# Performance work log

Hardware: AMD Instinct MI355X
Metric: run time of the kernel (lower is better)

## Reference

```python
import jax, jax.numpy as jnp
import numpy as np

N, E, DIN, H0, H1, HEADS = 50000, 600000, 128, 64, 64, 4
NEG_SLOPE = 0.2
BN_EPS = 1e-5


def setup_inputs() -> dict:
    key = jax.random.key(0)
    ks = iter(jax.random.split(key, 40))
    def p(shape, s=0.05):
        return jax.random.normal(next(ks), shape, jnp.float32) * s
    inp = {}
    inp['x'] = jax.random.normal(next(ks), (N, DIN), jnp.float32)
    inp['edge_index'] = jax.random.randint(next(ks), (2, E), 0, N, dtype=jnp.int32)
    inp['gcn1_w'] = p((DIN, H0)); inp['gcn1_b'] = p((H0,))
    inp['gcn2_w'] = p((H0, H1)); inp['gcn2_b'] = p((H1,))
    inp['gat1_w'] = p((DIN, HEADS * H0))
    inp['gat1_asrc'] = p((HEADS, H0)); inp['gat1_adst'] = p((HEADS, H0))
    inp['gat1_b'] = p((HEADS * H0,))
    inp['gat2_w'] = p((HEADS * H0, H1))
    inp['gat2_asrc'] = p((1, H1)); inp['gat2_adst'] = p((1, H1))
    inp['gat2_b'] = p((H1,))
    inp['sage1_wl'] = p((DIN, H0)); inp['sage1_bl'] = p((H0,)); inp['sage1_wr'] = p((DIN, H0))
    inp['sage2_wl'] = p((H0, H1)); inp['sage2_bl'] = p((H1,)); inp['sage2_wr'] = p((H0, H1))
    inp['bn_gcn_g'] = jnp.ones((H1,), jnp.float32); inp['bn_gcn_b'] = jnp.zeros((H1,), jnp.float32)
    inp['bn_gat_g'] = jnp.ones((H1,), jnp.float32); inp['bn_gat_b'] = jnp.zeros((H1,), jnp.float32)
    inp['bn_sage_g'] = jnp.ones((H1,), jnp.float32); inp['bn_sage_b'] = jnp.zeros((H1,), jnp.float32)
    inp['fc1_w'] = p((3 * H1, H1)); inp['fc1_b'] = p((H1,))
    inp['fc2_w'] = p((H1, 2)); inp['fc2_b'] = p((2,))
    return inp


def _gcn(x, w, b, src, dst, n):
    h = x @ w
    loop = jnp.arange(n)
    s = jnp.concatenate([src, loop]); d = jnp.concatenate([dst, loop])
    deg = jax.ops.segment_sum(jnp.ones(d.shape, h.dtype), d, n)
    dinv = jax.lax.rsqrt(jnp.maximum(deg, 1.0))  # deg >= 1 due to self-loops
    norm = dinv[s] * dinv[d]
    out = jax.ops.segment_sum(h[s] * norm[:, None], d, n)
    return out + b


def _gat(x, w, asrc, adst, b, src, dst, n, heads, outc, concat):
    # GATConv with self-loops; per-destination softmax over incoming edges
    h = (x @ w).reshape(n, heads, outc)
    loop = jnp.arange(n)
    s = jnp.concatenate([src, loop]); d = jnp.concatenate([dst, loop])
    a_s = jnp.einsum('nhc,hc->nh', h, asrc)
    a_d = jnp.einsum('nhc,hc->nh', h, adst)
    e = a_s[s] + a_d[d]                           # [Etot, H]
    e = jnp.where(e > 0, e, NEG_SLOPE * e)        # leaky relu
    emax = jax.ops.segment_max(e, d, n)           # every node has a self-loop
    ex = jnp.exp(e - emax[d])
    denom = jax.ops.segment_sum(ex, d, n)
    alpha = ex / (denom[d] + 1e-16)               # [Etot, H]
    out = jax.ops.segment_sum(h[s] * alpha[:, :, None], d, n)  # [n, H, C]
    out = out.reshape(n, heads * outc) if concat else out.mean(axis=1)
    return out + b


def _sage(x, wl, bl, wr, src, dst, n):
    # SAGEConv (mean aggr): lin_l(mean_j x_j) + lin_r(x_i)
    deg = jax.ops.segment_sum(jnp.ones(src.shape, x.dtype), dst, n)
    agg = jax.ops.segment_sum(x[src], dst, n) / jnp.maximum(deg, 1.0)[:, None]
    return agg @ wl + bl + x @ wr


def _bn(x, g, b):
    m = x.mean(0)
    v = x.var(0)
    return (x - m) * jax.lax.rsqrt(v + BN_EPS) * g + b


def reference(x, edge_index, gcn1_w, gcn1_b, gcn2_w, gcn2_b,
              gat1_w, gat1_asrc, gat1_adst, gat1_b,
              gat2_w, gat2_asrc, gat2_adst, gat2_b,
              sage1_wl, sage1_bl, sage1_wr, sage2_wl, sage2_bl, sage2_wr,
              bn_gcn_g, bn_gcn_b, bn_gat_g, bn_gat_b, bn_sage_g, bn_sage_b,
              fc1_w, fc1_b, fc2_w, fc2_b):
    src, dst = edge_index[0], edge_index[1]
    n = x.shape[0]
    g = jax.nn.relu(_gcn(x, gcn1_w, gcn1_b, src, dst, n))
    g = _bn(jax.nn.relu(_gcn(g, gcn2_w, gcn2_b, src, dst, n)), bn_gcn_g, bn_gcn_b)
    a = jax.nn.elu(_gat(x, gat1_w, gat1_asrc, gat1_adst, gat1_b, src, dst, n, HEADS, H0, True))
    a = _bn(jax.nn.elu(_gat(a, gat2_w, gat2_asrc, gat2_adst, gat2_b, src, dst, n, 1, H1, False)), bn_gat_g, bn_gat_b)
    s = jax.nn.relu(_sage(x, sage1_wl, sage1_bl, sage1_wr, src, dst, n))
    s = _bn(jax.nn.relu(_sage(s, sage2_wl, sage2_bl, sage2_wr, src, dst, n)), bn_sage_g, bn_sage_b)
    out = jnp.concatenate([g, a, s], axis=-1)
    h = jax.nn.relu(out @ fc1_w + fc1_b)
    return h @ fc2_w + fc2_b
```

## Files before the change

kernel.cpp:

```cpp
#include <hip/hip_runtime.h>
#include <math.h>

#define NEG_SLOPE 0.2f
#define BN_EPS 1e-5f

typedef short short8 __attribute__((ext_vector_type(8)));
typedef float floatx16 __attribute__((ext_vector_type(16)));

__device__ __forceinline__ float d_leaky(float x){ return x > 0.f ? x : NEG_SLOPE * x; }
__device__ __forceinline__ float d_elu(float x){ return x > 0.f ? x : expm1f(x); }

__device__ __forceinline__ unsigned short f2bf_rne(float f){
  unsigned int u = __float_as_uint(f);
  unsigned int r = (u + 0x7fffu + ((u >> 16) & 1u)) >> 16;
  return (unsigned short)r;
}
__device__ __forceinline__ float bf2f(unsigned short h){ return __uint_as_float((unsigned int)h << 16); }
__device__ __forceinline__ float2 bf2x(unsigned int u){
  float2 r;
  r.x = __uint_as_float(u << 16);
  r.y = __uint_as_float(u & 0xffff0000u);
  return r;
}

__device__ __forceinline__ float wave_sum(float v){
  #pragma unroll
  for (int off = 32; off > 0; off >>= 1) v += __shfl_xor(v, off, 64);
  return v;
}
__device__ __forceinline__ int wave_scan_incl(int v, int lane){
  #pragma unroll
  for (int off = 1; off < 64; off <<= 1){
    int u = __shfl_up(v, off, 64);
    if (lane >= off) v += u;
  }
  return v;
}

__global__ void k_count(const int* __restrict__ dst, int* __restrict__ deg, int E){
  int e = blockIdx.x * blockDim.x + threadIdx.x;
  if (e < E) atomicAdd(&deg[dst[e]], 1);
}

__global__ __launch_bounds__(256) void k_scan_a(const int* __restrict__ deg, int* __restrict__ bsum, int n){
  int t = threadIdx.x;
  int base = blockIdx.x * 1024 + t * 4;
  int d0=0,d1=0,d2=0,d3=0;
  if (base + 3 < n){ int4 v = *(const int4*)(deg + base); d0=v.x; d1=v.y; d2=v.z; d3=v.w; }
  else {
    if (base   < n) d0 = deg[base];
    if (base+1 < n) d1 = deg[base+1];
    if (base+2 < n) d2 = deg[base+2];
    if (base+3 < n) d3 = deg[base+3];
  }
  int s = d0+d1+d2+d3;
  __shared__ int wsm[4];
  int lane = t & 63, w = t >> 6;
  int incl = wave_scan_incl(s, lane);
  if (lane == 63) wsm[w] = incl;
  __syncthreads();
  if (t == 0) bsum[blockIdx.x] = wsm[0]+wsm[1]+wsm[2]+wsm[3];
}

__global__ void k_scan_b(int* __restrict__ bsum, int* __restrict__ rowp, int nb, int n){
  int t = threadIdx.x;
  int v = (t < nb) ? bsum[t] : 0;
  int incl = wave_scan_incl(v, t);
  if (t < nb) bsum[t] = incl - v;
  if (t == 63) rowp[n] = incl;
}

__global__ __launch_bounds__(256) void k_scan_c(const int* __restrict__ deg, const int* __restrict__ bsum,
                                                int* __restrict__ rowp, float* __restrict__ dinv,
                                                float* __restrict__ sdinv, int n){
  int t = threadIdx.x;
  int base = blockIdx.x * 1024 + t * 4;
  int d0=0,d1=0,d2=0,d3=0;
  if (base + 3 < n){ int4 v = *(const int4*)(deg + base); d0=v.x; d1=v.y; d2=v.z; d3=v.w; }
  else {
    if (base   < n) d0 = deg[base];
    if (base+1 < n) d1 = deg[base+1];
    if (base+2 < n) d2 = deg[base+2];
    if (base+3 < n) d3 = deg[base+3];
  }
  int s = d0+d1+d2+d3;
  __shared__ int wsm[4];
  int lane = t & 63, w = t >> 6;
  int incl = wave_scan_incl(s, lane);
  if (lane == 63) wsm[w] = incl;
  __syncthreads();
  int woff = 0;
  #pragma unroll
  for (int j = 0; j < 4; j++) if (j < w) woff += wsm[j];
  int r = bsum[blockIdx.x] + woff + incl - s;
  int dd[4] = {d0,d1,d2,d3};
  #pragma unroll
  for (int j = 0; j < 4; j++){
    int i = base + j;
    if (i < n){
      rowp[i] = r;
      dinv[i] = rsqrtf((float)(dd[j] + 1));
      sdinv[i] = 1.0f / fmaxf((float)dd[j], 1.0f);
    }
    r += dd[j];
  }
}

__global__ void k_scatter(const int* __restrict__ src, const int* __restrict__ dst,
                          const int* __restrict__ rowp, int* __restrict__ fill,
                          int* __restrict__ colv, int* __restrict__ dstv, int E){
  int e = blockIdx.x * blockDim.x + threadIdx.x;
  if (e < E){
    int d = dst[e];
    int pos = rowp[d] + atomicAdd(&fill[d], 1);
    colv[pos] = src[e];
    dstv[pos] = d;
  }
}

__global__ void k_asplit(const float* __restrict__ a, unsigned short* __restrict__ h,
                         unsigned short* __restrict__ l, int total){
  int i = blockIdx.x * blockDim.x + threadIdx.x;
  if (i < total){
    float v = a[i];
    unsigned short hh = f2bf_rne(v);
    h[i] = hh;
    l[i] = f2bf_rne(v - bf2f(hh));
  }
}

struct WDesc { const float* w; unsigned short* th; unsigned short* tl; int K; int Nc; int perm; };
struct WPack { WDesc d[8]; };
__global__ void k_wsplit(WPack p){
  WDesc w = p.d[blockIdx.y];
  int total = w.K * w.Nc;
  for (int i = blockIdx.x * blockDim.x + threadIdx.x; i < total; i += gridDim.x * blockDim.x){
    int k = i / w.Nc, n = i % w.Nc;
    int kd = (w.perm == 1) ? ((k & 63) * 4 + (k >> 6)) : k;
    int nd = (w.perm == 2) ? (((n & 63) << 2) | (n >> 6)) : n;
    float v = w.w[i];
    unsigned short h = f2bf_rne(v);
    w.th[(size_t)nd * w.K + kd] = h;
    w.tl[(size_t)nd * w.K + kd] = f2bf_rne(v - bf2f(h));
  }
}

__device__ __forceinline__ void gemm_term(floatx16& acc0, floatx16& acc1,
    const unsigned short* __restrict__ Ah, const unsigned short* __restrict__ Al,
    const unsigned short* __restrict__ Bh, const unsigned short* __restrict__ Bl,
    int K, int lda, int arow, int lr, int ko8){
  const unsigned short* ap  = Ah + (size_t)arow * lda + ko8;
  const unsigned short* alp = Al ? Al + (size_t)arow * lda + ko8 : nullptr;
  const unsigned short* bh0 = Bh + (size_t)lr * K + ko8;
  const unsigned short* bl0 = Bl + (size_t)lr * K + ko8;
  const unsigned short* bh1 = bh0 + (size_t)32 * K;
  const unsigned short* bl1 = bl0 + (size_t)32 * K;
  for (int k0 = 0; k0 < K; k0 += 16){
    short8 a  = *(const short8*)(ap + k0);
    short8 h0 = *(const short8*)(bh0 + k0);
    short8 l0 = *(const short8*)(bl0 + k0);
    short8 h1 = *(const short8*)(bh1 + k0);
    short8 l1 = *(const short8*)(bl1 + k0);
    if (alp){
      short8 a2 = *(const short8*)(alp + k0);
      acc0 = __builtin_amdgcn_mfma_f32_32x32x16_bf16(a2, h0, acc0, 0, 0, 0);
      acc1 = __builtin_amdgcn_mfma_f32_32x32x16_bf16(a2, h1, acc1, 0, 0, 0);
    }
    acc0 = __builtin_amdgcn_mfma_f32_32x32x16_bf16(a, l0, acc0, 0, 0, 0);
    acc0 = __builtin_amdgcn_mfma_f32_32x32x16_bf16(a, h0, acc0, 0, 0, 0);
    acc1 = __builtin_amdgcn_mfma_f32_32x32x16_bf16(a, l1, acc1, 0, 0, 0);
    acc1 = __builtin_amdgcn_mfma_f32_32x32x16_bf16(a, h1, acc1, 0, 0, 0);
  }
}

struct BDesc {
  const unsigned short *A1h, *A1l, *B1h, *B1l;
  const unsigned short *A2h, *A2l, *B2h, *B2l;
  int K1, lda1, K2, lda2;
  const float* bias;
  unsigned short* out; int ldc, coloff, act;
  const float* fc2w; const float* fc2b; float* outf;
};
struct BPack { BDesc d[3]; };
__global__ __launch_bounds__(256) void k_gemm_b(BPack p, int M){
  BDesc d = p.d[blockIdx.y];
  int wave = threadIdx.x >> 6, lane = threadIdx.x & 63;
  int m0 = blockIdx.x * 128 + wave * 32;
  int lr = lane & 31;
  int ko8 = (lane >> 5) * 8;
  floatx16 acc0 = {0,0,0,0,0,0,0,0,0,0,0,0,0,0,0,0};
  floatx16 acc1 = {0,0,0,0,0,0,0,0,0,0,0,0,0,0,0,0};
  int arow = m0 + lr; if (arow >= M) arow = M - 1;
  gemm_term(acc0, acc1, d.A1h, d.A1l, d.B1h, d.B1l, d.K1, d.lda1, arow, lr, ko8);
  if (d.K2) gemm_term(acc0, acc1, d.A2h, d.A2l, d.B2h, d.B2l, d.K2, d.lda2, arow, lr, ko8);
  int col0 = lr, col1 = lr + 32;
  float bias0 = d.bias ? d.bias[col0] : 0.f;
  float bias1 = d.bias ? d.bias[col1] : 0.f;
  float w00 = 0.f, w01 = 0.f, w10 = 0.f, w11 = 0.f;
  if (d.fc2w){
    w00 = d.fc2w[col0 * 2 + 0]; w01 = d.fc2w[col0 * 2 + 1];
    w10 = d.fc2w[col1 * 2 + 0]; w11 = d.fc2w[col1 * 2 + 1];
  }
  int rbase = m0 + 4 * (lane >> 5);
  #pragma unroll
  for (int reg = 0; reg < 16; reg++){
    int row = rbase + (reg & 3) + 8 * (reg >> 2);
    float v0 = acc0[reg] + bias0;
    float v1 = acc1[reg] + bias1;
    if (d.act){ v0 = fmaxf(v0, 0.f); v1 = fmaxf(v1, 0.f); }
    if (d.out && row < M){
      d.out[(size_t)row * d.ldc + d.coloff + col0] = f2bf_rne(v0);
      d.out[(size_t)row * d.ldc + d.coloff + col1] = f2bf_rne(v1);
    }
    if (d.fc2w){
      float p0 = v0 * w00 + v1 * w10;
      float p1 = v0 * w01 + v1 * w11;
      #pragma unroll
      for (int off = 16; off > 0; off >>= 1){
        p0 += __shfl_xor(p0, off, 64);
        p1 += __shfl_xor(p1, off, 64);
      }
      if ((lane & 31) == 0 && row < M){
        d.outf[(size_t)row * 2 + 0] = p0 + d.fc2b[0];
        d.outf[(size_t)row * 2 + 1] = p1 + d.fc2b[1];
      }
    }
  }
}

__global__ __launch_bounds__(256) void k_gemm320(
    const unsigned short* __restrict__ Ah, const unsigned short* __restrict__ Al,
    const unsigned short* __restrict__ Bh, const unsigned short* __restrict__ Bl,
    unsigned short* __restrict__ C1, unsigned short* __restrict__ C2, int M)
{
  const int K = 128;
  int wave = threadIdx.x >> 6, lane = threadIdx.x & 63;
  int m0 = blockIdx.x * 128 + wave * 32;
  int n0 = blockIdx.y * 64;
  int lr = lane & 31;
  int ko8 = (lane >> 5) * 8;
  floatx16 acc0 = {0,0,0,0,0,0,0,0,0,0,0,0,0,0,0,0};
  floatx16 acc1 = {0,0,0,0,0,0,0,0,0,0,0,0,0,0,0,0};
  int arow = m0 + lr; if (arow >= M) arow = M - 1;
  const unsigned short* ap_h = Ah + (size_t)arow * K + ko8;
  const unsigned short* ap_l = Al + (size_t)arow * K + ko8;
  const unsigned short* bp_h0 = Bh + (size_t)(n0 + lr) * K + ko8;
  const unsigned short* bp_l0 = Bl + (size_t)(n0 + lr) * K + ko8;
  const unsigned short* bp_h1 = bp_h0 + (size_t)32 * K;
  const unsigned short* bp_l1 = bp_l0 + (size_t)32 * K;
  for (int k0 = 0; k0 < K; k0 += 16){
    short8 a_h  = *(const short8*)(ap_h + k0);
    short8 a_l  = *(const short8*)(ap_l + k0);
    short8 b_h0 = *(const short8*)(bp_h0 + k0);
    short8 b_l0 = *(const short8*)(bp_l0 + k0);
    short8 b_h1 = *(const short8*)(bp_h1 + k0);
    short8 b_l1 = *(const short8*)(bp_l1 + k0);
    acc0 = __builtin_amdgcn_mfma_f32_32x32x16_bf16(a_l, b_h0, acc0, 0, 0, 0);
    acc0 = __builtin_amdgcn_mfma_f32_32x32x16_bf16(a_h, b_l0, acc0, 0, 0, 0);
    acc0 = __builtin_amdgcn_mfma_f32_32x32x16_bf16(a_h, b_h0, acc0, 0, 0, 0);
    acc1 = __builtin_amdgcn_mfma_f32_32x32x16_bf16(a_l, b_h1, acc1, 0, 0, 0);
    acc1 = __builtin_amdgcn_mfma_f32_32x32x16_bf16(a_h, b_l1, acc1, 0, 0, 0);
    acc1 = __builtin_amdgcn_mfma_f32_32x32x16_bf16(a_h, b_h1, acc1, 0, 0, 0);
  }
  int col0 = n0 + lr, col1 = col0 + 32;
  unsigned short* Cp; int ld, c0, c1;
  if (col0 >= 256){ Cp = C2; ld = 64; c0 = col0 - 256; c1 = col1 - 256; }
  else { Cp = C1; ld = 256; c0 = col0; c1 = col1; }
  int rbase = m0 + 4 * (lane >> 5);
  #pragma unroll
  for (int reg = 0; reg < 16; reg++){
    int row = rbase + (reg & 3) + 8 * (reg >> 2);
    if (row >= M) continue;
    Cp[(size_t)row * ld + c0] = f2bf_rne(acc0[reg]);
    Cp[(size_t)row * ld + c1] = f2bf_rne(acc1[reg]);
  }
}

__global__ __launch_bounds__(256) void k_gat_attn4(
    const unsigned short* __restrict__ h, const float* __restrict__ asrc,
    const float* __restrict__ adst, float* __restrict__ a_s, float* __restrict__ a_d, int n){
  int node = blockIdx.x * 4 + (threadIdx.x >> 6);
  int c = threadIdx.x & 63;
  if (node >= n) return;
  uint2 u = *(const uint2*)(h + (size_t)node * 256 + c * 4);
  float2 p0 = bf2x(u.x), p1 = bf2x(u.y);
  float s0 = wave_sum(p0.x * asrc[c]);
  float s1 = wave_sum(p0.y * asrc[64 + c]);
  float s2 = wave_sum(p1.x * asrc[128 + c]);
  float s3 = wave_sum(p1.y * asrc[192 + c]);
  float d0 = wave_sum(p0.x * adst[c]);
  float d1 = wave_sum(p0.y * adst[64 + c]);
  float d2 = wave_sum(p1.x * adst[128 + c]);
  float d3 = wave_sum(p1.y * adst[192 + c]);
  if (c == 0){
    *(float4*)(a_s + (size_t)node * 4) = make_float4(s0, s1, s2, s3);
    *(float4*)(a_d + (size_t)node * 4) = make_float4(d0, d1, d2, d3);
  }
}

__global__ __launch_bounds__(256) void k_gat_attn1(
    const unsigned short* __restrict__ h, int ld, const float* __restrict__ asrc,
    const float* __restrict__ adst, float* __restrict__ a_s, float* __restrict__ a_d, int n){
  int node = blockIdx.x * 4 + (threadIdx.x >> 6);
  int c = threadIdx.x & 63;
  if (node >= n) return;
  float v = bf2f(h[(size_t)node * ld + c]);
  float s = wave_sum(v * asrc[c]);
  float d = wave_sum(v * adst[c]);
  if (c == 0){ a_s[node] = s; a_d[node] = d; }
}

__global__ void k_edge_w4(const int* __restrict__ colv, const int* __restrict__ dstv,
                          const float* __restrict__ a_s, const float* __restrict__ a_d,
                          unsigned short* __restrict__ w4b, int E){
  int i = blockIdx.x * blockDim.x + threadIdx.x;
  if (i >= E) return;
  float4 s4 = *(const float4*)(a_s + (size_t)colv[i] * 4);
  float4 d4 = *(const float4*)(a_d + (size_t)dstv[i] * 4);
  float w0 = __expf(d_leaky(s4.x + d4.x));
  float w1 = __expf(d_leaky(s4.y + d4.y));
  float w2 = __expf(d_leaky(s4.z + d4.z));
  float w3 = __expf(d_leaky(s4.w + d4.w));
  uint2 q;
  q.x = (unsigned int)f2bf_rne(w0) | ((unsigned int)f2bf_rne(w1) << 16);
  q.y = (unsigned int)f2bf_rne(w2) | ((unsigned int)f2bf_rne(w3) << 16);
  *(uint2*)(w4b + (size_t)i * 4) = q;
}

__global__ void k_edge_w1(const int* __restrict__ colv, const int* __restrict__ dstv,
                          const float* __restrict__ a_s, const float* __restrict__ a_d,
                          float* __restrict__ w1, int E){
  int i = blockIdx.x * blockDim.x + threadIdx.x;
  if (i >= E) return;
  w1[i] = __expf(d_leaky(a_s[colv[i]] + a_d[dstv[i]]));
}

__global__ __launch_bounds__(256) void k_l1agg(
    const unsigned short* __restrict__ gath, const unsigned short* __restrict__ xh,
    const unsigned short* __restrict__ g1h,
    const int* __restrict__ rowp, const int* __restrict__ colv,
    const unsigned short* __restrict__ w4b,
    const float* __restrict__ a_s, const float* __restrict__ a_d,
    const float* __restrict__ gat1_b, const float* __restrict__ gcn1_b,
    const float* __restrict__ dinv, const float* __restrict__ sdinv,
    unsigned short* __restrict__ oh, unsigned short* __restrict__ g2h,
    unsigned short* __restrict__ aggXh, int n)
{
  int node = blockIdx.x * 4 + (threadIdx.x >> 6);
  int c = threadIdx.x & 63;
  if (node >= n) return;
  float4 asn = *(const float4*)(a_s + (size_t)node * 4);
  float4 adn = *(const float4*)(a_d + (size_t)node * 4);
  float ws0 = __expf(d_leaky(asn.x + adn.x));
  float ws1 = __expf(d_leaky(asn.y + adn.y));
  float ws2 = __expf(d_leaky(asn.z + adn.z));
  float ws3 = __expf(d_leaky(asn.w + adn.w));
  uint2 su = *(const uint2*)(gath + (size_t)node * 256 + c * 4);
  float2 sp0 = bf2x(su.x), sp1 = bf2x(su.y);
  float den0 = ws0, den1 = ws1, den2 = ws2, den3 = ws3;
  float acc0 = ws0 * sp0.x, acc1 = ws1 * sp0.y, acc2 = ws2 * sp1.x, acc3 = ws3 * sp1.y;
  float di = dinv[node];
  float gacc = di * bf2f(g1h[(size_t)node * 64 + c]);
  float sx0 = 0.f, sx1 = 0.f;
  int b = rowp[node], e = rowp[node + 1];
  for (int i = b; i < e; i += 8){
    int idx[8]; float mm[8]; int s[8];
    #pragma unroll
    for (int j = 0; j < 8; j++){
      int t = i + j;
      mm[j] = (t < e) ? 1.f : 0.f;
      idx[j] = (t < e) ? t : (e - 1);
    }
    #pragma unroll
    for (int j = 0; j < 8; j++) s[j] = colv[idx[j]];
    uint2 wq[8];
    #pragma unroll
    for (int j = 0; j < 8; j++) wq[j] = *(const uint2*)(w4b + (size_t)idx[j] * 4);
    uint2 hv[8];
    #pragma unroll
    for (int j = 0; j < 8; j++) hv[j] = *(const uint2*)(gath + (size_t)s[j] * 256 + c * 4);
    unsigned int hx[8];
    #pragma unroll
    for (int j = 0; j < 8; j++) hx[j] = *(const unsigned int*)(xh + (size_t)s[j] * 128 + c * 2);
    unsigned short hg[8];
    #pragma unroll
    for (int j = 0; j < 8; j++) hg[j] = g1h[(size_t)s[j] * 64 + c];
    float wd[8];
    #pragma unroll
    for (int j = 0; j < 8; j++) wd[j] = dinv[s[j]];
    #pragma unroll
    for (int j = 0; j < 8; j++){
      float m = mm[j];
      float2 w01 = bf2x(wq[j].x), w23 = bf2x(wq[j].y);
      float w0 = m * w01.x, w1 = m * w01.y, w2 = m * w23.x, w3 = m * w23.y;
      float2 a = bf2x(hv[j].x), bb = bf2x(hv[j].y);
      den0 += w0; den1 += w1; den2 += w2; den3 += w3;
      acc0 += w0 * a.x;  acc1 += w1 * a.y;
      acc2 += w2 * bb.x; acc3 += w3 * bb.y;
      gacc += m * wd[j] * bf2f(hg[j]);
      float2 p = bf2x(hx[j]);
      sx0 += m * p.x; sx1 += m * p.y;
    }
  }
  float v0 = d_elu(acc0 / (den0 + 1e-16f) + gat1_b[c]);
  float v1 = d_elu(acc1 / (den1 + 1e-16f) + gat1_b[64 + c]);
  float v2 = d_elu(acc2 / (den2 + 1e-16f) + gat1_b[128 + c]);
  float v3 = d_elu(acc3 / (den3 + 1e-16f) + gat1_b[192 + c]);
  uint2 ohv;
  ohv.x = (unsigned int)f2bf_rne(v0) | ((unsigned int)f2bf_rne(v1) << 16);
  ohv.y = (unsigned int)f2bf_rne(v2) | ((unsigned int)f2bf_rne(v3) << 16);
  *(uint2*)(oh + (size_t)node * 256 + c * 4) = ohv;
  g2h[(size_t)node * 64 + c] = f2bf_rne(fmaxf(di * gacc + gcn1_b[c], 0.f));
  float sd = sdinv[node];
  *(unsigned int*)(aggXh + (size_t)node * 128 + c * 2) =
      (unsigned int)f2bf_rne(sx0 * sd) | ((unsigned int)f2bf_rne(sx1 * sd) << 16);
}

__global__ __launch_bounds__(256) void k_f2(
    const unsigned short* __restrict__ m192,
    const int* __restrict__ rowp, const int* __restrict__ colv,
    const float* __restrict__ w1, const float* __restrict__ a_s, const float* __restrict__ a_d,
    const float* __restrict__ dinv, const float* __restrict__ sdinv,
    const float* __restrict__ gat2_b, const float* __restrict__ gcn2_b,
    unsigned short* __restrict__ cat,
    unsigned short* __restrict__ aggSh,
    int n){
  int node = blockIdx.x * 4 + (threadIdx.x >> 6);
  int c = threadIdx.x & 63;
  if (node >= n) return;
  float di = dinv[node];
  const unsigned short* srow = m192 + (size_t)node * 192;
  float tden = __expf(d_leaky(a_s[node] + a_d[node]));
  float tacc = tden * bf2f(srow[c]);
  float gacc = di * bf2f(srow[64 + c]);
  float sacc = 0.f;
  int b = rowp[node], e = rowp[node + 1];
  for (int i = b; i < e; i += 8){
    int idx[8]; float mm[8]; int s[8];
    #pragma unroll
    for (int j = 0; j < 8; j++){
      int t = i + j;
      mm[j] = (t < e) ? 1.f : 0.f;
      idx[j] = (t < e) ? t : (e - 1);
    }
    #pragma unroll
    for (int j = 0; j < 8; j++) s[j] = colv[idx[j]];
    float w[8];
    #pragma unroll
    for (int j = 0; j < 8; j++) w[j] = w1[idx[j]] * mm[j];
    unsigned short ht[8], hg[8], hs[8];
    #pragma unroll
    for (int j = 0; j < 8; j++){
      const unsigned short* r = m192 + (size_t)s[j] * 192;
      ht[j] = r[c]; hg[j] = r[64 + c]; hs[j] = r[128 + c];
    }
    float wd[8];
    #pragma unroll
    for (int j = 0; j < 8; j++) wd[j] = dinv[s[j]];
    #pragma unroll
    for (int j = 0; j < 8; j++){
      tden += w[j]; tacc += w[j] * bf2f(ht[j]);
      gacc += mm[j] * wd[j] * bf2f(hg[j]);
      sacc += mm[j] * bf2f(hs[j]);
    }
  }
  cat[(size_t)node * 192 + 64 + c] = f2bf_rne(d_elu(tacc / (tden + 1e-16f) + gat2_b[c]));
  cat[(size_t)node * 192 + c] = f2bf_rne(fmaxf(di * gacc + gcn2_b[c], 0.f));
  aggSh[(size_t)node * 64 + c] = f2bf_rne(sacc * sdinv[node]);
}

__global__ void k_bn_stats3(const unsigned short* __restrict__ x,
                            float* __restrict__ bnGCN, float* __restrict__ bnGAT,
                            float* __restrict__ bnSAGE, int n){
  int seg = blockIdx.y;
  float* sums = (seg == 0) ? bnGCN : (seg == 1) ? bnGAT : bnSAGE;
  int co = seg * 64;
  int c = threadIdx.x & 63;
  int rl = threadIdx.x >> 6;
  float s = 0.f, q = 0.f;
  for (int r = blockIdx.x * 4 + rl; r < n; r += gridDim.x * 4){
    float v = bf2f(x[(size_t)r * 192 + co + c]);
    s += v; q += v * v;
  }
  __shared__ float ls[4][64], lq[4][64];
  ls[rl][c] = s; lq[rl][c] = q;
  __syncthreads();
  if (rl == 0){
    s = ls[0][c] + ls[1][c] + ls[2][c] + ls[3][c];
    q = lq[0][c] + lq[1][c] + lq[2][c] + lq[3][c];
    atomicAdd(&sums[c], s);
    atomicAdd(&sums[64 + c], q);
  }
}

__global__ __launch_bounds__(256) void k_bnfold(
    const float* __restrict__ bnGCN, const float* __restrict__ bnGAT, const float* __restrict__ bnSAGE,
    const float* __restrict__ gg, const float* __restrict__ gb,
    const float* __restrict__ ag, const float* __restrict__ ab,
    const float* __restrict__ sg, const float* __restrict__ sb,
    const float* __restrict__ w, const float* __restrict__ wb, float nf,
    unsigned short* __restrict__ fwh, unsigned short* __restrict__ fwl, float* __restrict__ fb)
{
  int tid = threadIdx.x;
  auto st = [&](int c, float& s, float& t){
    int cc = c & 63;
    const float *bn, *g, *b;
    if (c < 64){ bn = bnGCN; g = gg; b = gb; }
    else if (c < 128){ bn = bnGAT; g = ag; b = ab; }
    else { bn = bnSAGE; g = sg; b = sb; }
    float m = bn[cc] / nf;
    float var = bn[64 + cc] / nf - m * m;
    float inv = rsqrtf(var + BN_EPS);
    s = inv * g[cc];
    t = b[cc] - m * inv * g[cc];
  };
  if (tid < 64){
    float acc = wb[tid];
    for (int c = 0; c < 192; c++){
      float s, t; st(c, s, t);
      acc += t * w[c * 64 + tid];
    }
    fb[tid] = acc;
  }
  for (int i = tid; i < 192 * 64; i += 256){
    int c = i >> 6, nn = i & 63;
    float s, t; st(c, s, t);
    float v = s * w[i];
    unsigned short hh = f2bf_rne(v);
    fwh[nn * 192 + c] = hh;
    fwl[nn * 192 + c] = f2bf_rne(v - bf2f(hh));
  }
}

extern "C" void kernel_launch(void* const* d_in, const int* in_sizes, int n_in,
                              void* d_out, int out_size, void* d_ws, size_t ws_size,
                              hipStream_t stream){
  (void)n_in; (void)out_size; (void)ws_size;
  const float* x        = (const float*)d_in[0];
  const int*   ei       = (const int*)  d_in[1];
  const float* gcn1_w   = (const float*)d_in[2];
  const float* gcn1_b   = (const float*)d_in[3];
  const float* gcn2_w   = (const float*)d_in[4];
  const float* gcn2_b   = (const float*)d_in[5];
  const float* gat1_w   = (const float*)d_in[6];
  const float* gat1_as  = (const float*)d_in[7];
  const float* gat1_ad  = (const float*)d_in[8];
  const float* gat1_b   = (const float*)d_in[9];
  const float* gat2_w   = (const float*)d_in[10];
  const float* gat2_as  = (const float*)d_in[11];
  const float* gat2_ad  = (const float*)d_in[12];
  const float* gat2_b   = (const float*)d_in[13];
  const float* sage1_wl = (const float*)d_in[14];
  const float* sage1_bl = (const float*)d_in[15];
  const float* sage1_wr = (const float*)d_in[16];
  const float* sage2_wl = (const float*)d_in[17];
  const float* sage2_bl = (const float*)d_in[18];
  const float* sage2_wr = (const float*)d_in[19];
  const float* bn_gcn_g = (const float*)d_in[20];
  const float* bn_gcn_b = (const float*)d_in[21];
  const float* bn_gat_g = (const float*)d_in[22];
  const float* bn_gat_b = (const float*)d_in[23];
  const float* bn_sage_g= (const float*)d_in[24];
  const float* bn_sage_b= (const float*)d_in[25];
  const float* fc1_w    = (const float*)d_in[26];
  const float* fc1_b    = (const float*)d_in[27];
  const float* fc2_w    = (const float*)d_in[28];
  const float* fc2_b    = (const float*)d_in[29];
  float* out = (float*)d_out;

  const int N = in_sizes[0] / 128;
  const int E = in_sizes[1] / 2;
  const int* src = ei;
  const int* dst = ei + E;
  const int nb = (N + 1023) / 1024;

  char* ws = (char*)d_ws;
  size_t off = 0;
  auto alloc = [&](size_t bytes) -> void* {
    void* p = ws + off;
    off = (off + bytes + 255) & ~(size_t)255;
    return p;
  };
  char* zbase = (char*)alloc(0);
  int*   deg   = (int*)  alloc((size_t)N * 4);
  int*   fill  = (int*)  alloc((size_t)N * 4);
  float* bnA   = (float*)alloc(128 * 4);
  float* bnB   = (float*)alloc(128 * 4);
  float* bnC   = (float*)alloc(128 * 4);
  size_t zbytes = (size_t)((char*)alloc(0) - zbase);
  int*   rowp  = (int*)  alloc((size_t)(N + 1) * 4);
  int*   colv  = (int*)  alloc((size_t)E * 4);
  int*   dstv  = (int*)  alloc((size_t)E * 4);
  int*   bsum  = (int*)  alloc(64 * 4);
  float* dinv  = (float*)alloc((size_t)N * 4);
  float* sdinv = (float*)alloc((size_t)N * 4);
  float* as1   = (float*)alloc((size_t)N * 4 * 4);
  float* ad1   = (float*)alloc((size_t)N * 4 * 4);
  float* as2   = (float*)alloc((size_t)N * 4);
  float* ad2   = (float*)alloc((size_t)N * 4);
  unsigned short* w4b = (unsigned short*)alloc((size_t)E * 4 * 2);
  float* w1    = (float*)alloc((size_t)E * 4);
  unsigned short* xh    = (unsigned short*)alloc((size_t)N * 128 * 2);
  unsigned short* xl    = (unsigned short*)alloc((size_t)N * 128 * 2);
  unsigned short* gath  = (unsigned short*)alloc((size_t)N * 256 * 2);
  unsigned short* oh    = (unsigned short*)alloc((size_t)N * 256 * 2);
  unsigned short* g1h   = (unsigned short*)alloc((size_t)N * 64 * 2);
  unsigned short* g2h   = (unsigned short*)alloc((size_t)N * 64 * 2);
  unsigned short* aggXh = (unsigned short*)alloc((size_t)N * 128 * 2);
  unsigned short* aggSh = (unsigned short*)alloc((size_t)N * 64 * 2);
  unsigned short* m192  = (unsigned short*)alloc((size_t)N * 192 * 2);
  unsigned short* cath  = (unsigned short*)alloc((size_t)N * 192 * 2);
  unsigned short* b320h = (unsigned short*)alloc((size_t)320 * 128 * 2);
  unsigned short* b320l = (unsigned short*)alloc((size_t)320 * 128 * 2);
  unsigned short* gcn2h = (unsigned short*)alloc((size_t)64 * 64 * 2);
  unsigned short* gcn2l = (unsigned short*)alloc((size_t)64 * 64 * 2);
  unsigned short* gat2h = (unsigned short*)alloc((size_t)64 * 256 * 2);
  unsigned short* gat2l = (unsigned short*)alloc((size_t)64 * 256 * 2);
  unsigned short* s1wlh = (unsigned short*)alloc((size_t)64 * 128 * 2);
  unsigned short* s1wll = (unsigned short*)alloc((size_t)64 * 128 * 2);
  unsigned short* s1wrh = (unsigned short*)alloc((size_t)64 * 128 * 2);
  unsigned short* s1wrl = (unsigned short*)alloc((size_t)64 * 128 * 2);
  unsigned short* s2wlh = (unsigned short*)alloc((size_t)64 * 64 * 2);
  unsigned short* s2wll = (unsigned short*)alloc((size_t)64 * 64 * 2);
  unsigned short* s2wrh = (unsigned short*)alloc((size_t)64 * 64 * 2);
  unsigned short* s2wrl = (unsigned short*)alloc((size_t)64 * 64 * 2);
  unsigned short* fwh   = (unsigned short*)alloc((size_t)64 * 192 * 2);
  unsigned short* fwl   = (unsigned short*)alloc((size_t)64 * 192 * 2);
  float* fb             = (float*)alloc(64 * 4);

  hipMemsetAsync(zbase, 0, zbytes, stream);

  k_count <<<(E + 255) / 256, 256, 0, stream>>>(dst, deg, E);
  k_scan_a<<<nb, 256, 0, stream>>>(deg, bsum, N);
  k_scan_b<<<1, 64, 0, stream>>>(bsum, rowp, nb, N);
  k_scan_c<<<nb, 256, 0, stream>>>(deg, bsum, rowp, dinv, sdinv, N);
  k_scatter<<<(E + 255) / 256, 256, 0, stream>>>(src, dst, rowp, fill, colv, dstv, E);

  {
    WPack p;
    p.d[0] = {gat1_w, b320h, b320l, 128, 256, 2};
    p.d[1] = {gcn1_w, b320h + 256 * 128, b320l + 256 * 128, 128, 64, 0};
    p.d[2] = {gat2_w, gat2h, gat2l, 256, 64, 1};
    p.d[3] = {sage1_wl, s1wlh, s1wll, 128, 64, 0};
    p.d[4] = {sage1_wr, s1wrh, s1wrl, 128, 64, 0};
    p.d[5] = {sage2_wl, s2wlh, s2wll, 64, 64, 0};
    p.d[6] = {sage2_wr, s2wrh, s2wrl, 64, 64, 0};
    p.d[7] = {gcn2_w, gcn2h, gcn2l, 64, 64, 0};
    dim3 g(32, 8);
    k_wsplit<<<g, 256, 0, stream>>>(p);
  }
  k_asplit<<<(N * 128 + 255) / 256, 256, 0, stream>>>(x, xh, xl, N * 128);

  const int gx = (N + 127) / 128;
  const int gn = (N + 3) / 4;

  {
    dim3 g(gx, 5);
    k_gemm320<<<g, 256, 0, stream>>>(xh, xl, b320h, b320l, gath, g1h, N);
  }
  k_gat_attn4<<<gn, 256, 0, stream>>>(gath, gat1_as, gat1_ad, as1, ad1, N);
  k_edge_w4<<<(E + 255) / 256, 256, 0, stream>>>(colv, dstv, as1, ad1, w4b, E);
  k_l1agg<<<gn, 256, 0, stream>>>(gath, xh, g1h, rowp, colv, w4b, as1, ad1,
                                  gat1_b, gcn1_b, dinv, sdinv, oh, g2h, aggXh, N);

  {
    BPack p;
    p.d[0] = {oh, nullptr, gat2h, gat2l, nullptr, nullptr, nullptr, nullptr,
              256, 256, 0, 0, nullptr, m192, 192, 0, 0, nullptr, nullptr, nullptr};
    p.d[1] = {g2h, nullptr, gcn2h, gcn2l, nullptr, nullptr, nullptr, nullptr,
              64, 64, 0, 0, nullptr, m192, 192, 64, 0, nullptr, nullptr, nullptr};
    p.d[2] = {aggXh, nullptr, s1wlh, s1wll, xh, xl, s1wrh, s1wrl,
              128, 128, 128, 128, sage1_bl, m192, 192, 128, 1, nullptr, nullptr, nullptr};
    dim3 g(gx, 3);
    k_gemm_b<<<g, 256, 0, stream>>>(p, N);
  }
  k_gat_attn1<<<gn, 256, 0, stream>>>(m192, 192, gat2_as, gat2_ad, as2, ad2, N);
  k_edge_w1<<<(E + 255) / 256, 256, 0, stream>>>(colv, dstv, as2, ad2, w1, E);
  k_f2<<<gn, 256, 0, stream>>>(m192, rowp, colv, w1, as2, ad2, dinv, sdinv,
                               gat2_b, gcn2_b, cath, aggSh, N);

  {
    BPack p;
    p.d[0] = {aggSh, nullptr, s2wlh, s2wll, m192 + 128, nullptr, s2wrh, s2wrl,
              64, 64, 64, 192, sage2_bl, cath, 192, 128, 1, nullptr, nullptr, nullptr};
    p.d[1] = p.d[0]; p.d[2] = p.d[0];
    dim3 g(gx, 1);
    k_gemm_b<<<g, 256, 0, stream>>>(p, N);
  }

  {
    dim3 g(128, 3);
    k_bn_stats3<<<g, 256, 0, stream>>>(cath, bnB, bnA, bnC, N);
  }
  k_bnfold<<<1, 256, 0, stream>>>(bnB, bnA, bnC,
                                  bn_gcn_g, bn_gcn_b, bn_gat_g, bn_gat_b, bn_sage_g, bn_sage_b,
                                  fc1_w, fc1_b, (float)N, fwh, fwl, fb);

  {
    BPack p;
    p.d[0] = {cath, nullptr, fwh, fwl, nullptr, nullptr, nullptr, nullptr,
              192, 192, 0, 0, fb, nullptr, 64, 0, 1, fc2_w, fc2_b, out};
    p.d[1] = p.d[0]; p.d[2] = p.d[0];
    dim3 g(gx, 1);
    k_gemm_b<<<g, 256, 0, stream>>>(p, N);
  }
}
```

Baseline: 633.3 us.

## Fuse small kernels: scan, asplit, GAT2 attention, edge weights, BN fold

Cuts the launch count in several places. The single-block scan step moves into k_scan_c, which also seeds fill with row offsets so the scatter no longer reads rowp. The x bf16 split becomes an extra slot of k_wsplit. The GAT layer-2 attention dot products are computed in the GEMM epilogue through the fc2 path, and the edge weights are computed inline in k_f2 instead of in a separate edge kernel with its own buffer. BN statistics and the fold are merged with a last-block-done atomic counter. The trade-offs are more exp work inside the aggregation loop and extra global atomics and fences.

```diff
diff --git a/kernel.cpp b/kernel.cpp
--- a/kernel.cpp
+++ b/kernel.cpp
@@ -37,8 +37,11 @@
   return v;
 }
 
-__global__ void k_count(const int* __restrict__ dst, int* __restrict__ deg, int E){
+__global__ void k_count(const int* __restrict__ dst, int* __restrict__ deg, int E,
+                        const float* __restrict__ g2as, const float* __restrict__ g2ad,
+                        float* __restrict__ aw2){
   int e = blockIdx.x * blockDim.x + threadIdx.x;
+  if (e < 64){ aw2[e * 2 + 0] = g2as[e]; aw2[e * 2 + 1] = g2ad[e]; }
   if (e < E) atomicAdd(&deg[dst[e]], 1);
 }
 
@@ -62,18 +65,18 @@
   if (t == 0) bsum[blockIdx.x] = wsm[0]+wsm[1]+wsm[2]+wsm[3];
 }
 
-__global__ void k_scan_b(int* __restrict__ bsum, int* __restrict__ rowp, int nb, int n){
+__global__ __launch_bounds__(256) void k_scan_c(const int* __restrict__ deg, const int* __restrict__ bsum,
+                                                int* __restrict__ rowp, int* __restrict__ fill,
+                                                float* __restrict__ dinv,
+                                                float* __restrict__ sdinv, int n, int nb){
+  __shared__ int sbx[2];
   int t = threadIdx.x;
-  int v = (t < nb) ? bsum[t] : 0;
-  int incl = wave_scan_incl(v, t);
-  if (t < nb) bsum[t] = incl - v;
-  if (t == 63) rowp[n] = incl;
-}
-
-__global__ __launch_bounds__(256) void k_scan_c(const int* __restrict__ deg, const int* __restrict__ bsum,
-                                                int* __restrict__ rowp, float* __restrict__ dinv,
-                                                float* __restrict__ sdinv, int n){
-  int t = threadIdx.x;
+  if (t < 64){
+    int v = (t < nb) ? bsum[t] : 0;
+    int incl = wave_scan_incl(v, t);
+    if (t == (int)blockIdx.x) sbx[0] = incl - v;
+    if (t == 63) sbx[1] = incl;
+  }
   int base = blockIdx.x * 1024 + t * 4;
   int d0=0,d1=0,d2=0,d3=0;
   if (base + 3 < n){ int4 v = *(const int4*)(deg + base); d0=v.x; d1=v.y; d2=v.z; d3=v.w; }
@@ -92,48 +95,48 @@
   int woff = 0;
   #pragma unroll
   for (int j = 0; j < 4; j++) if (j < w) woff += wsm[j];
-  int r = bsum[blockIdx.x] + woff + incl - s;
+  int r = sbx[0] + woff + incl - s;
   int dd[4] = {d0,d1,d2,d3};
   #pragma unroll
   for (int j = 0; j < 4; j++){
     int i = base + j;
     if (i < n){
       rowp[i] = r;
+      fill[i] = r;
       dinv[i] = rsqrtf((float)(dd[j] + 1));
       sdinv[i] = 1.0f / fmaxf((float)dd[j], 1.0f);
     }
     r += dd[j];
   }
+  if (blockIdx.x == 0 && t == 0) rowp[n] = sbx[1];
 }
 
 __global__ void k_scatter(const int* __restrict__ src, const int* __restrict__ dst,
-                          const int* __restrict__ rowp, int* __restrict__ fill,
+                          int* __restrict__ fill,
                           int* __restrict__ colv, int* __restrict__ dstv, int E){
   int e = blockIdx.x * blockDim.x + threadIdx.x;
   if (e < E){
     int d = dst[e];
-    int pos = rowp[d] + atomicAdd(&fill[d], 1);
+    int pos = atomicAdd(&fill[d], 1);
     colv[pos] = src[e];
     dstv[pos] = d;
   }
 }
 
-__global__ void k_asplit(const float* __restrict__ a, unsigned short* __restrict__ h,
-                         unsigned short* __restrict__ l, int total){
-  int i = blockIdx.x * blockDim.x + threadIdx.x;
-  if (i < total){
-    float v = a[i];
-    unsigned short hh = f2bf_rne(v);
-    h[i] = hh;
-    l[i] = f2bf_rne(v - bf2f(hh));
-  }
-}
-
 struct WDesc { const float* w; unsigned short* th; unsigned short* tl; int K; int Nc; int perm; };
-struct WPack { WDesc d[8]; };
+struct WPack { WDesc d[9]; };
 __global__ void k_wsplit(WPack p){
   WDesc w = p.d[blockIdx.y];
   int total = w.K * w.Nc;
+  if (w.perm == 3){
+    for (int i = blockIdx.x * blockDim.x + threadIdx.x; i < total; i += gridDim.x * blockDim.x){
+      float v = w.w[i];
+      unsigned short h = f2bf_rne(v);
+      w.th[i] = h;
+      w.tl[i] = f2bf_rne(v - bf2f(h));
+    }
+    return;
+  }
   for (int i = blockIdx.x * blockDim.x + threadIdx.x; i < total; i += gridDim.x * blockDim.x){
     int k = i / w.Nc, n = i % w.Nc;
     int kd = (w.perm == 1) ? ((k & 63) * 4 + (k >> 6)) : k;
@@ -196,10 +199,11 @@
   int col0 = lr, col1 = lr + 32;
   float bias0 = d.bias ? d.bias[col0] : 0.f;
   float bias1 = d.bias ? d.bias[col1] : 0.f;
-  float w00 = 0.f, w01 = 0.f, w10 = 0.f, w11 = 0.f;
+  float w00 = 0.f, w01 = 0.f, w10 = 0.f, w11 = 0.f, fb0 = 0.f, fb1 = 0.f;
   if (d.fc2w){
     w00 = d.fc2w[col0 * 2 + 0]; w01 = d.fc2w[col0 * 2 + 1];
     w10 = d.fc2w[col1 * 2 + 0]; w11 = d.fc2w[col1 * 2 + 1];
+    if (d.fc2b){ fb0 = d.fc2b[0]; fb1 = d.fc2b[1]; }
   }
   int rbase = m0 + 4 * (lane >> 5);
   #pragma unroll
@@ -221,8 +225,8 @@
         p1 += __shfl_xor(p1, off, 64);
       }
       if ((lane & 31) == 0 && row < M){
-        d.outf[(size_t)row * 2 + 0] = p0 + d.fc2b[0];
-        d.outf[(size_t)row * 2 + 1] = p1 + d.fc2b[1];
+        d.outf[(size_t)row * 2 + 0] = p0 + fb0;
+        d.outf[(size_t)row * 2 + 1] = p1 + fb1;
       }
     }
   }
@@ -298,18 +302,6 @@
   }
 }
 
-__global__ __launch_bounds__(256) void k_gat_attn1(
-    const unsigned short* __restrict__ h, int ld, const float* __restrict__ asrc,
-    const float* __restrict__ adst, float* __restrict__ a_s, float* __restrict__ a_d, int n){
-  int node = blockIdx.x * 4 + (threadIdx.x >> 6);
-  int c = threadIdx.x & 63;
-  if (node >= n) return;
-  float v = bf2f(h[(size_t)node * ld + c]);
-  float s = wave_sum(v * asrc[c]);
-  float d = wave_sum(v * adst[c]);
-  if (c == 0){ a_s[node] = s; a_d[node] = d; }
-}
-
 __global__ void k_edge_w4(const int* __restrict__ colv, const int* __restrict__ dstv,
                           const float* __restrict__ a_s, const float* __restrict__ a_d,
                           unsigned short* __restrict__ w4b, int E){
@@ -325,14 +317,6 @@
   q.x = (unsigned int)f2bf_rne(w0) | ((unsigned int)f2bf_rne(w1) << 16);
   q.y = (unsigned int)f2bf_rne(w2) | ((unsigned int)f2bf_rne(w3) << 16);
   *(uint2*)(w4b + (size_t)i * 4) = q;
-}
-
-__global__ void k_edge_w1(const int* __restrict__ colv, const int* __restrict__ dstv,
-                          const float* __restrict__ a_s, const float* __restrict__ a_d,
-                          float* __restrict__ w1, int E){
-  int i = blockIdx.x * blockDim.x + threadIdx.x;
-  if (i >= E) return;
-  w1[i] = __expf(d_leaky(a_s[colv[i]] + a_d[dstv[i]]));
 }
 
 __global__ __launch_bounds__(256) void k_l1agg(
@@ -419,7 +403,7 @@
 __global__ __launch_bounds__(256) void k_f2(
     const unsigned short* __restrict__ m192,
     const int* __restrict__ rowp, const int* __restrict__ colv,
-    const float* __restrict__ w1, const float* __restrict__ a_s, const float* __restrict__ a_d,
+    const float* __restrict__ as2ad2,
     const float* __restrict__ dinv, const float* __restrict__ sdinv,
     const float* __restrict__ gat2_b, const float* __restrict__ gcn2_b,
     unsigned short* __restrict__ cat,
@@ -430,7 +414,8 @@
   if (node >= n) return;
   float di = dinv[node];
   const unsigned short* srow = m192 + (size_t)node * 192;
-  float tden = __expf(d_leaky(a_s[node] + a_d[node]));
+  float adn = as2ad2[node * 2 + 1];
+  float tden = __expf(d_leaky(as2ad2[node * 2 + 0] + adn));
   float tacc = tden * bf2f(srow[c]);
   float gacc = di * bf2f(srow[64 + c]);
   float sacc = 0.f;
@@ -447,7 +432,7 @@
     for (int j = 0; j < 8; j++) s[j] = colv[idx[j]];
     float w[8];
     #pragma unroll
-    for (int j = 0; j < 8; j++) w[j] = w1[idx[j]] * mm[j];
+    for (int j = 0; j < 8; j++) w[j] = mm[j] * __expf(d_leaky(as2ad2[(size_t)s[j] * 2] + adn));
     unsigned short ht[8], hg[8], hs[8];
     #pragma unroll
     for (int j = 0; j < 8; j++){
@@ -469,9 +454,16 @@
   aggSh[(size_t)node * 64 + c] = f2bf_rne(sacc * sdinv[node]);
 }
 
-__global__ void k_bn_stats3(const unsigned short* __restrict__ x,
-                            float* __restrict__ bnGCN, float* __restrict__ bnGAT,
-                            float* __restrict__ bnSAGE, int n){
+__global__ __launch_bounds__(256) void k_bn_stats_fold(
+    const unsigned short* __restrict__ x,
+    float* __restrict__ bnGCN, float* __restrict__ bnGAT, float* __restrict__ bnSAGE,
+    const float* __restrict__ gg, const float* __restrict__ gb,
+    const float* __restrict__ ag, const float* __restrict__ ab,
+    const float* __restrict__ sg, const float* __restrict__ sb,
+    const float* __restrict__ w, const float* __restrict__ wb, float nf,
+    unsigned short* __restrict__ fwh, unsigned short* __restrict__ fwl, float* __restrict__ fb,
+    int* __restrict__ done, int nblocks, int n)
+{
   int seg = blockIdx.y;
   float* sums = (seg == 0) ? bnGCN : (seg == 1) ? bnGAT : bnSAGE;
   int co = seg * 64;
@@ -491,44 +483,51 @@
     atomicAdd(&sums[c], s);
     atomicAdd(&sums[64 + c], q);
   }
-}
-
-__global__ __launch_bounds__(256) void k_bnfold(
-    const float* __restrict__ bnGCN, const float* __restrict__ bnGAT, const float* __restrict__ bnSAGE,
-    const float* __restrict__ gg, const float* __restrict__ gb,
-    const float* __restrict__ ag, const float* __restrict__ ab,
-    const float* __restrict__ sg, const float* __restrict__ sb,
-    const float* __restrict__ w, const float* __restrict__ wb, float nf,
-    unsigned short* __restrict__ fwh, unsigned short* __restrict__ fwl, float* __restrict__ fb)
-{
+  __syncthreads();
+  __shared__ int lastflag;
+  if (threadIdx.x == 0){
+    __threadfence();
+    int old = atomicAdd(done, 1);
+    lastflag = (old == nblocks - 1);
+  }
+  __syncthreads();
+  if (!lastflag) return;
+  __threadfence();
+  __shared__ float sbn[3][128];
+  for (int i = threadIdx.x; i < 384; i += 256){
+    float* p = (i < 128) ? bnGCN : (i < 256) ? bnGAT : bnSAGE;
+    sbn[i >> 7][i & 127] = atomicAdd(&p[i & 127], 0.0f);
+  }
+  __syncthreads();
   int tid = threadIdx.x;
-  auto st = [&](int c, float& s, float& t){
-    int cc = c & 63;
-    const float *bn, *g, *b;
-    if (c < 64){ bn = bnGCN; g = gg; b = gb; }
-    else if (c < 128){ bn = bnGAT; g = ag; b = ab; }
-    else { bn = bnSAGE; g = sg; b = sb; }
-    float m = bn[cc] / nf;
-    float var = bn[64 + cc] / nf - m * m;
+  auto st = [&](int c2, float& sc, float& tc){
+    int cc = c2 & 63;
+    int sg2 = c2 >> 6;
+    const float *g, *b;
+    if (sg2 == 0){ g = gg; b = gb; }
+    else if (sg2 == 1){ g = ag; b = ab; }
+    else { g = sg; b = sb; }
+    float m = sbn[sg2][cc] / nf;
+    float var = sbn[sg2][64 + cc] / nf - m * m;
     float inv = rsqrtf(var + BN_EPS);
-    s = inv * g[cc];
-    t = b[cc] - m * inv * g[cc];
+    sc = inv * g[cc];
+    tc = b[cc] - m * inv * g[cc];
   };
   if (tid < 64){
     float acc = wb[tid];
-    for (int c = 0; c < 192; c++){
-      float s, t; st(c, s, t);
-      acc += t * w[c * 64 + tid];
+    for (int c2 = 0; c2 < 192; c2++){
+      float sc, tc; st(c2, sc, tc);
+      acc += tc * w[c2 * 64 + tid];
     }
     fb[tid] = acc;
   }
   for (int i = tid; i < 192 * 64; i += 256){
-    int c = i >> 6, nn = i & 63;
-    float s, t; st(c, s, t);
-    float v = s * w[i];
+    int c2 = i >> 6, nn = i & 63;
+    float sc, tc; st(c2, sc, tc);
+    float v = sc * w[i];
     unsigned short hh = f2bf_rne(v);
-    fwh[nn * 192 + c] = hh;
-    fwl[nn * 192 + c] = f2bf_rne(v - bf2f(hh));
+    fwh[nn * 192 + c2] = hh;
+    fwl[nn * 192 + c2] = f2bf_rne(v - bf2f(hh));
   }
 }
 
@@ -583,12 +582,13 @@
   };
   char* zbase = (char*)alloc(0);
   int*   deg   = (int*)  alloc((size_t)N * 4);
-  int*   fill  = (int*)  alloc((size_t)N * 4);
   float* bnA   = (float*)alloc(128 * 4);
   float* bnB   = (float*)alloc(128 * 4);
   float* bnC   = (float*)alloc(128 * 4);
+  int*   done  = (int*)  alloc(4);
   size_t zbytes = (size_t)((char*)alloc(0) - zbase);
   int*   rowp  = (int*)  alloc((size_t)(N + 1) * 4);
+  int*   fill  = (int*)  alloc((size_t)N * 4);
   int*   colv  = (int*)  alloc((size_t)E * 4);
   int*   dstv  = (int*)  alloc((size_t)E * 4);
   int*   bsum  = (int*)  alloc(64 * 4);
@@ -596,10 +596,9 @@
   float* sdinv = (float*)alloc((size_t)N * 4);
   float* as1   = (float*)alloc((size_t)N * 4 * 4);
   float* ad1   = (float*)alloc((size_t)N * 4 * 4);
-  float* as2   = (float*)alloc((size_t)N * 4);
-  float* ad2   = (float*)alloc((size_t)N * 4);
+  float* as2ad2= (float*)alloc((size_t)N * 2 * 4);
+  float* aw2   = (float*)alloc(128 * 4);
   unsigned short* w4b = (unsigned short*)alloc((size_t)E * 4 * 2);
-  float* w1    = (float*)alloc((size_t)E * 4);
   unsigned short* xh    = (unsigned short*)alloc((size_t)N * 128 * 2);
   unsigned short* xl    = (unsigned short*)alloc((size_t)N * 128 * 2);
   unsigned short* gath  = (unsigned short*)alloc((size_t)N * 256 * 2);
@@ -630,11 +629,10 @@
 
   hipMemsetAsync(zbase, 0, zbytes, stream);
 
-  k_count <<<(E + 255) / 256, 256, 0, stream>>>(dst, deg, E);
+  k_count <<<(E + 255) / 256, 256, 0, stream>>>(dst, deg, E, gat2_as, gat2_ad, aw2);
   k_scan_a<<<nb, 256, 0, stream>>>(deg, bsum, N);
-  k_scan_b<<<1, 64, 0, stream>>>(bsum, rowp, nb, N);
-  k_scan_c<<<nb, 256, 0, stream>>>(deg, bsum, rowp, dinv, sdinv, N);
-  k_scatter<<<(E + 255) / 256, 256, 0, stream>>>(src, dst, rowp, fill, colv, dstv, E);
+  k_scan_c<<<nb, 256, 0, stream>>>(deg, bsum, rowp, fill, dinv, sdinv, N, nb);
+  k_scatter<<<(E + 255) / 256, 256, 0, stream>>>(src, dst, fill, colv, dstv, E);
 
   {
     WPack p;
@@ -646,10 +644,10 @@
     p.d[5] = {sage2_wl, s2wlh, s2wll, 64, 64, 0};
     p.d[6] = {sage2_wr, s2wrh, s2wrl, 64, 64, 0};
     p.d[7] = {gcn2_w, gcn2h, gcn2l, 64, 64, 0};
-    dim3 g(32, 8);
+    p.d[8] = {x, xh, xl, N, 128, 3};
+    dim3 g(1024, 9);
     k_wsplit<<<g, 256, 0, stream>>>(p);
   }
-  k_asplit<<<(N * 128 + 255) / 256, 256, 0, stream>>>(x, xh, xl, N * 128);
 
   const int gx = (N + 127) / 128;
   const int gn = (N + 3) / 4;
@@ -666,7 +664,7 @@
   {
     BPack p;
     p.d[0] = {oh, nullptr, gat2h, gat2l, nullptr, nullptr, nullptr, nullptr,
-              256, 256, 0, 0, nullptr, m192, 192, 0, 0, nullptr, nullptr, nullptr};
+              256, 256, 0, 0, nullptr, m192, 192, 0, 0, aw2, nullptr, as2ad2};
     p.d[1] = {g2h, nullptr, gcn2h, gcn2l, nullptr, nullptr, nullptr, nullptr,
               64, 64, 0, 0, nullptr, m192, 192, 64, 0, nullptr, nullptr, nullptr};
     p.d[2] = {aggXh, nullptr, s1wlh, s1wll, xh, xl, s1wrh, s1wrl,
@@ -674,9 +672,7 @@
     dim3 g(gx, 3);
     k_gemm_b<<<g, 256, 0, stream>>>(p, N);
   }
-  k_gat_attn1<<<gn, 256, 0, stream>>>(m192, 192, gat2_as, gat2_ad, as2, ad2, N);
-  k_edge_w1<<<(E + 255) / 256, 256, 0, stream>>>(colv, dstv, as2, ad2, w1, E);
-  k_f2<<<gn, 256, 0, stream>>>(m192, rowp, colv, w1, as2, ad2, dinv, sdinv,
+  k_f2<<<gn, 256, 0, stream>>>(m192, rowp, colv, as2ad2, dinv, sdinv,
                                gat2_b, gcn2_b, cath, aggSh, N);
 
   {
@@ -690,11 +686,12 @@
 
   {
     dim3 g(128, 3);
-    k_bn_stats3<<<g, 256, 0, stream>>>(cath, bnB, bnA, bnC, N);
-  }
-  k_bnfold<<<1, 256, 0, stream>>>(bnB, bnA, bnC,
-                                  bn_gcn_g, bn_gcn_b, bn_gat_g, bn_gat_b, bn_sage_g, bn_sage_b,
-                                  fc1_w, fc1_b, (float)N, fwh, fwl, fb);
+    k_bn_stats_fold<<<g, 256, 0, stream>>>(cath, bnB, bnA, bnC,
+                                           bn_gcn_g, bn_gcn_b, bn_gat_g, bn_gat_b,
+                                           bn_sage_g, bn_sage_b,
+                                           fc1_w, fc1_b, (float)N, fwh, fwl, fb,
+                                           done, 128 * 3, N);
+  }
 
   {
     BPack p;
```

New measurement: 622.1 us. No clear change (-1.8%).
